# Performance work log

Measured on AMD Instinct MI355X. Metric: run time of the kernel, lower is better.

Reference implementation:

```python
import jax, jax.numpy as jnp
import numpy as np

VOCAB = 10000
EMBED = 100
SEQ = 80
BATCH = 256
UNITS = 2048


def setup_inputs() -> dict:
    key = jax.random.key(0)
    ks = jax.random.split(key, 10)
    s = lambda fan_in: 1.0 / np.sqrt(fan_in)
    inputs = jax.random.randint(ks[0], (BATCH, SEQ), 0, VOCAB, dtype=jnp.int32)
    emb = jax.random.normal(ks[1], (VOCAB, EMBED), dtype=jnp.float32) * 0.05
    W0 = jax.random.normal(ks[2], (EMBED, UNITS), dtype=jnp.float32) * s(EMBED)
    U0 = jax.random.normal(ks[3], (UNITS, UNITS), dtype=jnp.float32) * s(UNITS)
    b0 = jnp.zeros((UNITS,), dtype=jnp.float32)
    W1 = jax.random.normal(ks[4], (UNITS, UNITS), dtype=jnp.float32) * s(UNITS)
    U1 = jax.random.normal(ks[5], (UNITS, UNITS), dtype=jnp.float32) * s(UNITS)
    b1 = jnp.zeros((UNITS,), dtype=jnp.float32)
    Wo = jax.random.normal(ks[6], (UNITS, 1), dtype=jnp.float32) * s(UNITS)
    bo = jnp.zeros((1,), dtype=jnp.float32)
    return {"inputs": inputs, "emb": emb, "W0": W0, "U0": U0, "b0": b0,
            "W1": W1, "U1": U1, "b1": b1, "Wo": Wo, "bo": bo}


def reference(inputs, emb, W0, U0, b0, W1, U1, b1, Wo, bo):
    # Embedding lookup: [B, T, E]
    x = emb[inputs]
    # time-major for scan: [T, B, E]
    xt = jnp.transpose(x, (1, 0, 2))
    B = inputs.shape[0]
    h0_init = jnp.zeros((B, U0.shape[0]), dtype=x.dtype)
    h1_init = jnp.zeros((B, U1.shape[0]), dtype=x.dtype)

    def step(carry, x_t):
        h0, h1 = carry
        # SimpleRNNCell: h' = tanh(x W + h U + b); dropout inactive (training=None)
        h0 = jnp.tanh(x_t @ W0 + h0 @ U0 + b0)
        h1 = jnp.tanh(h0 @ W1 + h1 @ U1 + b1)
        return (h0, h1), None

    (_, h1_final), _ = jax.lax.scan(step, (h0_init, h1_init), xt)
    logits = h1_final @ Wo + bo  # [B, 1]
    return jax.nn.sigmoid(logits)
```

## Files before the change

kernel.cpp:

```cpp
#include <hip/hip_runtime.h>


typedef _Float16 f16;
typedef _Float16 f16x2 __attribute__((ext_vector_type(2)));
typedef _Float16 f16x8 __attribute__((ext_vector_type(8)));
typedef float    f32x4 __attribute__((ext_vector_type(4)));

#define NWG    256
#define SEQ    80
#define EPAD   128
#define NKC0   68
#define NKC1   128

#define FLAGS_OFF   0
#define B0S_OFF     1024
#define B0S_SIZE    (2176 * 2048 * 2)
#define B1S_OFF     (B0S_OFF + B0S_SIZE)
#define B1S_SIZE    (4096 * 2048 * 2)
#define XP_OFF      (B1S_OFF + B1S_SIZE)
#define XP_SIZE     (SEQ * 256 * EPAD * 2)
#define H0_OFF      (XP_OFF + XP_SIZE)
#define HSLOT       (256 * 2048 * 2)
#define HSLOT_H     (256 * 2048)
#define WS_FULL     ((size_t)H0_OFF + (size_t)162 * HSLOT)
#define WS_MIN      ((size_t)H0_OFF + (size_t)6 * HSLOT)

__device__ __forceinline__ float tanh_fast(float x) {
  x = fminf(15.f, fmaxf(-15.f, x));
  float e = __expf(2.f * x);
  return (e - 1.f) * __builtin_amdgcn_rcpf(e + 1.f);
}

__device__ __forceinline__ f16x8 ldg16_coh(const f16* p) {
  f16x8 r;
  asm volatile("global_load_dwordx4 %0, %1, off sc0 sc1" : "=v"(r) : "v"(p));
  return r;
}
__device__ __forceinline__ f16x8 ldg16(const f16* p) {
  f16x8 r;
  asm volatile("global_load_dwordx4 %0, %1, off" : "=v"(r) : "v"(p));
  return r;
}
__device__ __forceinline__ void stg16_coh(f16* p, f16x8 v) {
  asm volatile("global_store_dwordx4 %0, %1, off sc0 sc1" :: "v"(p), "v"(v) : "memory");
}
#define VWAIT(name, n)                                                        \
__device__ __forceinline__ void name(f16x8 (&a)[4], f16x8 (&b)[4]) {          \
  asm volatile("s_waitcnt vmcnt(" #n ")"                                      \
    : "+v"(a[0]), "+v"(a[1]), "+v"(a[2]), "+v"(a[3]),                         \
      "+v"(b[0]), "+v"(b[1]), "+v"(b[2]), "+v"(b[3]) :: "memory");            \
}
VWAIT(vwait16, 16)
VWAIT(vwait8, 8)
VWAIT(vwait0, 0)

__device__ __forceinline__ void gbar(int* flags, int target) {
  asm volatile("s_waitcnt vmcnt(0)" ::: "memory");
  __syncthreads();
  if (threadIdx.x == 0)
    __hip_atomic_store(&flags[blockIdx.x], target, __ATOMIC_RELAXED,
                       __HIP_MEMORY_SCOPE_AGENT);
  if (threadIdx.x < NWG) {
    while (__hip_atomic_load(&flags[threadIdx.x], __ATOMIC_RELAXED,
                             __HIP_MEMORY_SCOPE_AGENT) < target)
      __builtin_amdgcn_s_sleep(2);
  }
  __syncthreads();
}

__global__ __launch_bounds__(256) void fmt_weights(
    const float* __restrict__ W0, const float* __restrict__ U0,
    const float* __restrict__ W1, const float* __restrict__ U1,
    char* __restrict__ ws)
{
  int frag = blockIdx.x * 4 + (threadIdx.x >> 6);
  int lane = threadIdx.x & 63, lr = lane & 15, lk = (lane >> 4) * 8;
  f16x8 h;
  f16* dst;
  if (frag < 32 * NKC0 * 4) {
    int slice = frag / (NKC0 * 4), rem = frag % (NKC0 * 4);
    int kcg = rem >> 2, n16 = rem & 3;
    int col = slice * 64 + n16 * 16 + lr;
#pragma unroll
    for (int j = 0; j < 8; ++j) {
      int k = kcg * 32 + lk + j;
      float v;
      if (k < 2048) v = U0[(size_t)k * 2048 + col];
      else { int e = k - 2048; v = (e < 100) ? W0[(size_t)e * 2048 + col] : 0.f; }
      h[j] = (f16)v;
    }
    dst = (f16*)(ws + B0S_OFF) + (size_t)frag * 512;
  } else {
    int fr = frag - 32 * NKC0 * 4;
    int slice = fr / (NKC1 * 4), rem = fr % (NKC1 * 4);
    int kcg = rem >> 2, n16 = rem & 3;
    int col = slice * 64 + n16 * 16 + lr;
#pragma unroll
    for (int j = 0; j < 8; ++j) {
      int k = kcg * 32 + lk + j;
      float v = (k < 2048) ? W1[(size_t)k * 2048 + col]
                           : U1[(size_t)(k - 2048) * 2048 + col];
      h[j] = (f16)v;
    }
    dst = (f16*)(ws + B1S_OFF) + (size_t)fr * 512;
  }
  *(f16x8*)(dst + lane * 8) = h;
}

__global__ __launch_bounds__(256) void embed_k(
    const int* __restrict__ inputs, const float* __restrict__ emb,
    char* __restrict__ ws)
{
  int r = blockIdx.x * 4 + (threadIdx.x >> 6);
  int lane = threadIdx.x & 63;
  int t = r >> 8, b = r & 255;
  int idx = inputs[b * SEQ + t];
  int e = lane * 2;
  f16x2 h;
  if (e < 100) {
    const float* src = emb + (size_t)idx * 100 + e;
    h[0] = (f16)src[0]; h[1] = (f16)src[1];
  } else { h[0] = (f16)0.f; h[1] = (f16)0.f; }
  *(f16x2*)(ws + XP_OFF + ((size_t)r * EPAD + e) * 2) = h;
}

template <int NKC, bool L0T, bool COH>
__device__ __forceinline__ void ktile(
    const f16* __restrict__ Ab, const f16* __restrict__ Xp,
    const f16* __restrict__ bp, const size_t* aoff, const size_t* xoff,
    int kb, f32x4 (&acc)[4][4])
{
  f16x8 A[3][4], B[3][4];
  auto LD = [&](int kc, f16x8 (&a)[4], f16x8 (&b)[4]) {
#pragma unroll
    for (int cf = 0; cf < 4; ++cf)
      b[cf] = ldg16(bp + (size_t)kc * 2048 + cf * 512);
    int kk = kb + kc * 32;
    if (L0T && kk >= 2048) {
#pragma unroll
      for (int rf = 0; rf < 4; ++rf)
        a[rf] = ldg16(Xp + xoff[rf] + (kk - 2048));
    } else {
#pragma unroll
      for (int rf = 0; rf < 4; ++rf) {
        const f16* p = Ab + aoff[rf] + kk;
        if (COH) a[rf] = ldg16_coh(p); else a[rf] = ldg16(p);
      }
    }
  };
  auto ST = [&](f16x8 (&a)[4], f16x8 (&b)[4]) {
#pragma unroll
    for (int cf = 0; cf < 4; ++cf)
#pragma unroll
      for (int rf = 0; rf < 4; ++rf)
        acc[rf][cf] = __builtin_amdgcn_mfma_f32_16x16x32_f16(
            a[rf], b[cf], acc[rf][cf], 0, 0, 0);
  };

  LD(0, A[0], B[0]);
  if (NKC > 1) LD(1, A[1], B[1]);
#pragma unroll
  for (int kc = 0; kc < NKC; ++kc) {
    f16x8 (&a)[4] = A[kc % 3];
    f16x8 (&b)[4] = B[kc % 3];
    if (kc + 2 < NKC) { LD(kc + 2, A[(kc + 2) % 3], B[(kc + 2) % 3]); vwait16(a, b); }
    else if (kc + 1 < NKC) vwait8(a, b);
    else vwait0(a, b);
    ST(a, b);
  }
}

template <int NBUF, bool COH>
__global__ __launch_bounds__(512, 2) void rnn_persist(
    const float* __restrict__ b0v, const float* __restrict__ b1v,
    char* __restrict__ ws)
{
  __shared__ f32x4 red[8][8][64];
  __shared__ f16 T[64 * 64];

  const int bid = blockIdx.x;
  const int tid = threadIdx.x;
  const int wv = tid >> 6, lane = tid & 63;
  const int lr = lane & 15, lk = (lane >> 4) * 8;

  int* flags = (int*)(ws + FLAGS_OFF);
  f16* H0b = (f16*)(ws + H0_OFF);
  f16* H1b = H0b + (size_t)NBUF * HSLOT_H;
  const f16* Xp = (const f16*)(ws + XP_OFF);

  const bool isL0 = bid < 128;
  const int u = isL0 ? bid : bid - 128;
  const int cslice = (u & 7) * 4 + ((u >> 3) & 3);
  const int m0 = (u >> 5) * 64;
  const int n0 = cslice * 64;
  const f16* Bst = (const f16*)(ws + (isL0 ? B0S_OFF : B1S_OFF));
  const int kcgb = isL0 ? wv * 9 : wv * 16;
  const float* bias = isL0 ? b0v : b1v;

  const f16* bp = Bst + ((size_t)cslice * (isL0 ? NKC0 : NKC1) + kcgb) * 2048 + lane * 8;

  size_t aoff[4], xoff[4];
#pragma unroll
  for (int rf = 0; rf < 4; ++rf)
    aoff[rf] = (size_t)(m0 + rf * 16 + lr) * 2048 + lk;

  for (int p = 0; p <= 80; ++p) {
    const f16* Hr0 = H0b + (size_t)(p % NBUF) * HSLOT_H;
    const f16* Hr1 = H1b + (size_t)((p >= 1 ? (p - 1) % NBUF : 0)) * HSLOT_H;
    f16* Hw = isL0 ? H0b + (size_t)((p + 1) % NBUF) * HSLOT_H
                   : H1b + (size_t)(p % NBUF) * HSLOT_H;
    const bool active = isL0 ? (p < 80) : true;
    const bool fzero  = (!isL0) && (p == 0);

    f32x4 acc[4][4];
#pragma unroll
    for (int a = 0; a < 4; ++a)
#pragma unroll
      for (int b = 0; b < 4; ++b) acc[a][b] = {0.f, 0.f, 0.f, 0.f};

    if (active && !fzero) {
      if (isL0) {
#pragma unroll
        for (int rf = 0; rf < 4; ++rf)
          xoff[rf] = ((size_t)p * 256 + m0 + rf * 16 + lr) * EPAD + lk;
        if (wv < 7) ktile<9, true, COH>(Hr0, Xp, bp, aoff, xoff, wv * 288, acc);
        else        ktile<5, true, COH>(Hr0, Xp, bp, aoff, xoff, wv * 288, acc);
      } else {
        const f16* Ab = (wv < 4) ? Hr0 : Hr1;
        ktile<16, false, COH>(Ab, Xp, bp, aoff, xoff, (wv & 3) * 512, acc);
      }
    }

    if (active) {
#pragma unroll
      for (int t = 0; t < 2; ++t) {
        if (t) __syncthreads();
#pragma unroll
        for (int rr = 0; rr < 2; ++rr)
#pragma unroll
          for (int cf = 0; cf < 4; ++cf)
            red[wv][rr * 4 + cf][lane] = acc[2 * t + rr][cf];
        __syncthreads();
        {
          const int rf = 2 * t + (wv >> 2), cf = wv & 3;
          f32x4 s = red[0][wv][lane];
#pragma unroll
          for (int ow = 1; ow < 8; ++ow) s += red[ow][wv][lane];
          const int tcol = cf * 16 + lr;
          const float bv = bias[n0 + tcol];
          const int trow = rf * 16 + (lane >> 4) * 4;
#pragma unroll
          for (int r = 0; r < 4; ++r) {
            const float v = fzero ? 0.f : tanh_fast(s[r] + bv);
            T[(trow + r) * 64 + (tcol ^ (((trow + r) & 3) << 4))] = (f16)v;
          }
        }
      }
      __syncthreads();
      {
        const int row = tid >> 3, c8 = (tid & 7) * 8;
        f16x8 val = *(const f16x8*)(T + row * 64 + (c8 ^ ((row & 3) << 4)));
        stg16_coh(Hw + (size_t)(m0 + row) * 2048 + n0 + c8, val);
      }
    }
    if (p < 80) gbar(flags, p + 1);
  }
}

__global__ __launch_bounds__(256) void logits_k(
    const f16* __restrict__ h1, const float* __restrict__ Wo,
    const float* __restrict__ bo, float* __restrict__ out)
{
  int row = blockIdx.x * 4 + (threadIdx.x >> 6);
  int lane = threadIdx.x & 63;
  const f16* hr = h1 + (size_t)row * 2048;
  float s = 0.f;
#pragma unroll
  for (int it = 0; it < 4; ++it) {
    int k = it * 512 + lane * 8;
    f16x8 hv = *(const f16x8*)(hr + k);
    const float4* wp = (const float4*)(Wo + k);
    float4 w0 = wp[0], w1 = wp[1];
    s += (float)hv[0] * w0.x + (float)hv[1] * w0.y + (float)hv[2] * w0.z + (float)hv[3] * w0.w;
    s += (float)hv[4] * w1.x + (float)hv[5] * w1.y + (float)hv[6] * w1.z + (float)hv[7] * w1.w;
  }
#pragma unroll
  for (int off = 32; off > 0; off >>= 1) s += __shfl_down(s, off);
  if (lane == 0) out[row] = 1.f / (1.f + __expf(-(s + bo[0])));
}

extern "C" void kernel_launch(void* const* d_in, const int* in_sizes, int n_in,
                              void* d_out, int out_size, void* d_ws, size_t ws_size,
                              hipStream_t stream)
{
  (void)in_sizes; (void)n_in; (void)out_size;
  const int*   inputs = (const int*)d_in[0];
  const float* emb    = (const float*)d_in[1];
  const float* W0     = (const float*)d_in[2];
  const float* U0     = (const float*)d_in[3];
  const float* b0     = (const float*)d_in[4];
  const float* W1     = (const float*)d_in[5];
  const float* U1     = (const float*)d_in[6];
  const float* b1     = (const float*)d_in[7];
  const float* Wo     = (const float*)d_in[8];
  const float* bo     = (const float*)d_in[9];
  char* ws = (char*)d_ws;
  if (ws_size < WS_MIN) return;

  const bool full = (ws_size >= WS_FULL);
  const int  nbuf = full ? 81 : 3;

  hipMemsetAsync(ws + FLAGS_OFF, 0, 1024, stream);
  hipMemsetAsync(ws + H0_OFF, 0, HSLOT, stream);
  hipMemsetAsync(ws + H0_OFF + (size_t)nbuf * HSLOT, 0, HSLOT, stream);

  fmt_weights<<<6272, 256, 0, stream>>>(W0, U0, W1, U1, ws);
  embed_k<<<5120, 256, 0, stream>>>(inputs, emb, ws);
  if (full) rnn_persist<81, false><<<NWG, 512, 0, stream>>>(b0, b1, ws);
  else      rnn_persist<3,  true ><<<NWG, 512, 0, stream>>>(b0, b1, ws);

  const f16* h1f = (const f16*)(ws + H0_OFF + (size_t)nbuf * HSLOT
                                + (size_t)(80 % nbuf) * HSLOT);
  logits_k<<<64, 256, 0, stream>>>(h1f, Wo, bo, (float*)d_out);
}
```

Measured before the change: 2.875 ms.

## Keep per-workgroup weight slices resident in LDS and drop cross-wave reduction

Each workgroup now owns a 16-column output slice over the full K range and preloads its whole weight slice into 128 KB of shared memory once, instead of streaming weights from global memory every timestep. Each wave computes 32 batch rows over the full K, which removes the LDS cross-wave reduction and its extra barriers. The cost is that every workgroup reads the entire hidden state each step, so L2 traffic for activations rises. Outputs are written as scattered 2-byte coherent stores, and occupancy drops to one block per CU.

```diff
diff --git a/kernel.cpp b/kernel.cpp
--- a/kernel.cpp
+++ b/kernel.cpp
@@ -14,9 +14,9 @@
 
 #define FLAGS_OFF   0
 #define B0S_OFF     1024
-#define B0S_SIZE    (2176 * 2048 * 2)
+#define B0S_SIZE    (8704 * 1024)
 #define B1S_OFF     (B0S_OFF + B0S_SIZE)
-#define B1S_SIZE    (4096 * 2048 * 2)
+#define B1S_SIZE    (16384 * 1024)
 #define XP_OFF      (B1S_OFF + B1S_SIZE)
 #define XP_SIZE     (SEQ * 256 * EPAD * 2)
 #define H0_OFF      (XP_OFF + XP_SIZE)
@@ -44,14 +44,18 @@
 __device__ __forceinline__ void stg16_coh(f16* p, f16x8 v) {
   asm volatile("global_store_dwordx4 %0, %1, off sc0 sc1" :: "v"(p), "v"(v) : "memory");
 }
+__device__ __forceinline__ void stg2_coh(f16* p, f16 v) {
+  unsigned int w = (unsigned int)__builtin_bit_cast(unsigned short, v);
+  asm volatile("global_store_short %0, %1, off sc0 sc1" :: "v"(p), "v"(w) : "memory");
+}
 #define VWAIT(name, n)                                                        \
-__device__ __forceinline__ void name(f16x8 (&a)[4], f16x8 (&b)[4]) {          \
+__device__ __forceinline__ void name(f16x8 (&a)[2]) {                         \
   asm volatile("s_waitcnt vmcnt(" #n ")"                                      \
-    : "+v"(a[0]), "+v"(a[1]), "+v"(a[2]), "+v"(a[3]),                         \
-      "+v"(b[0]), "+v"(b[1]), "+v"(b[2]), "+v"(b[3]) :: "memory");            \
-}
-VWAIT(vwait16, 16)
-VWAIT(vwait8, 8)
+    : "+v"(a[0]), "+v"(a[1]) :: "memory");                                    \
+}
+VWAIT(vwait6, 6)
+VWAIT(vwait4, 4)
+VWAIT(vwait2, 2)
 VWAIT(vwait0, 0)
 
 __device__ __forceinline__ void gbar(int* flags, int target) {
@@ -77,13 +81,12 @@
   int lane = threadIdx.x & 63, lr = lane & 15, lk = (lane >> 4) * 8;
   f16x8 h;
   f16* dst;
-  if (frag < 32 * NKC0 * 4) {
-    int slice = frag / (NKC0 * 4), rem = frag % (NKC0 * 4);
-    int kcg = rem >> 2, n16 = rem & 3;
-    int col = slice * 64 + n16 * 16 + lr;
+  if (frag < 128 * NKC0) {
+    int slice = frag / NKC0, kc = frag % NKC0;
+    int col = slice * 16 + lr;
 #pragma unroll
     for (int j = 0; j < 8; ++j) {
-      int k = kcg * 32 + lk + j;
+      int k = kc * 32 + lk + j;
       float v;
       if (k < 2048) v = U0[(size_t)k * 2048 + col];
       else { int e = k - 2048; v = (e < 100) ? W0[(size_t)e * 2048 + col] : 0.f; }
@@ -91,18 +94,17 @@
     }
     dst = (f16*)(ws + B0S_OFF) + (size_t)frag * 512;
   } else {
-    int fr = frag - 32 * NKC0 * 4;
-    int slice = fr / (NKC1 * 4), rem = fr % (NKC1 * 4);
-    int kcg = rem >> 2, n16 = rem & 3;
-    int col = slice * 64 + n16 * 16 + lr;
+    int g2 = frag - 128 * NKC0;
+    int kc = g2 & 127;
+    int col = (g2 >> 7) * 16 + lr;
 #pragma unroll
     for (int j = 0; j < 8; ++j) {
-      int k = kcg * 32 + lk + j;
+      int k = kc * 32 + lk + j;
       float v = (k < 2048) ? W1[(size_t)k * 2048 + col]
                            : U1[(size_t)(k - 2048) * 2048 + col];
       h[j] = (f16)v;
     }
-    dst = (f16*)(ws + B1S_OFF) + (size_t)fr * 512;
+    dst = (f16*)(ws + B1S_OFF) + (size_t)g2 * 512;
   }
   *(f16x8*)(dst + lane * 8) = h;
 }
@@ -124,59 +126,43 @@
   *(f16x2*)(ws + XP_OFF + ((size_t)r * EPAD + e) * 2) = h;
 }
 
-template <int NKC, bool L0T, bool COH>
-__device__ __forceinline__ void ktile(
-    const f16* __restrict__ Ab, const f16* __restrict__ Xp,
-    const f16* __restrict__ bp, const size_t* aoff, const size_t* xoff,
-    int kb, f32x4 (&acc)[4][4])
-{
-  f16x8 A[3][4], B[3][4];
-  auto LD = [&](int kc, f16x8 (&a)[4], f16x8 (&b)[4]) {
-#pragma unroll
-    for (int cf = 0; cf < 4; ++cf)
-      b[cf] = ldg16(bp + (size_t)kc * 2048 + cf * 512);
-    int kk = kb + kc * 32;
-    if (L0T && kk >= 2048) {
-#pragma unroll
-      for (int rf = 0; rf < 4; ++rf)
-        a[rf] = ldg16(Xp + xoff[rf] + (kk - 2048));
-    } else {
-#pragma unroll
-      for (int rf = 0; rf < 4; ++rf) {
-        const f16* p = Ab + aoff[rf] + kk;
-        if (COH) a[rf] = ldg16_coh(p); else a[rf] = ldg16(p);
-      }
-    }
-  };
-  auto ST = [&](f16x8 (&a)[4], f16x8 (&b)[4]) {
-#pragma unroll
-    for (int cf = 0; cf < 4; ++cf)
-#pragma unroll
-      for (int rf = 0; rf < 4; ++rf)
-        acc[rf][cf] = __builtin_amdgcn_mfma_f32_16x16x32_f16(
-            a[rf], b[cf], acc[rf][cf], 0, 0, 0);
-  };
-
-  LD(0, A[0], B[0]);
-  if (NKC > 1) LD(1, A[1], B[1]);
-#pragma unroll
-  for (int kc = 0; kc < NKC; ++kc) {
-    f16x8 (&a)[4] = A[kc % 3];
-    f16x8 (&b)[4] = B[kc % 3];
-    if (kc + 2 < NKC) { LD(kc + 2, A[(kc + 2) % 3], B[(kc + 2) % 3]); vwait16(a, b); }
-    else if (kc + 1 < NKC) vwait8(a, b);
-    else vwait0(a, b);
-    ST(a, b);
-  }
-}
+#define KLOOP(NKC, A1, A2, O1, O2)                                            \
+  do {                                                                        \
+    f16x8 A_[4][2];                                                           \
+    auto LD = [&](int kc, f16x8 (&a)[2]) {                                    \
+      _Pragma("unroll")                                                       \
+      for (int mf = 0; mf < 2; ++mf) {                                        \
+        const f16* p = (kc < 64) ? (A1) + (O1)[mf] + (size_t)kc * 32          \
+                                 : (A2) + (O2)[mf] + (size_t)(kc - 64) * 32;  \
+        if (COH) a[mf] = ldg16_coh(p); else a[mf] = ldg16(p);                 \
+      }                                                                       \
+    };                                                                        \
+    auto STEP = [&](int kc, f16x8 (&a)[2]) {                                  \
+      f16x8 b = Bsh[kc * 64 + lane];                                          \
+      acc[0] = __builtin_amdgcn_mfma_f32_16x16x32_f16(a[0], b, acc[0], 0, 0, 0); \
+      acc[1] = __builtin_amdgcn_mfma_f32_16x16x32_f16(a[1], b, acc[1], 0, 0, 0); \
+    };                                                                        \
+    LD(0, A_[0]); LD(1, A_[1]); LD(2, A_[2]);                                 \
+    for (int kq = 0; kq < (NKC) / 4 - 1; ++kq) {                              \
+      const int k0 = kq * 4;                                                  \
+      LD(k0 + 3, A_[3]); vwait6(A_[0]); STEP(k0 + 0, A_[0]);                  \
+      LD(k0 + 4, A_[0]); vwait6(A_[1]); STEP(k0 + 1, A_[1]);                  \
+      LD(k0 + 5, A_[1]); vwait6(A_[2]); STEP(k0 + 2, A_[2]);                  \
+      LD(k0 + 6, A_[2]); vwait6(A_[3]); STEP(k0 + 3, A_[3]);                  \
+    }                                                                         \
+    LD((NKC) - 1, A_[3]);                                                     \
+    vwait6(A_[0]); STEP((NKC) - 4, A_[0]);                                    \
+    vwait4(A_[1]); STEP((NKC) - 3, A_[1]);                                    \
+    vwait2(A_[2]); STEP((NKC) - 2, A_[2]);                                    \
+    vwait0(A_[3]); STEP((NKC) - 1, A_[3]);                                    \
+  } while (0)
 
 template <int NBUF, bool COH>
-__global__ __launch_bounds__(512, 2) void rnn_persist(
+__global__ __launch_bounds__(512, 1) void rnn_persist(
     const float* __restrict__ b0v, const float* __restrict__ b1v,
     char* __restrict__ ws)
 {
-  __shared__ f32x4 red[8][8][64];
-  __shared__ f16 T[64 * 64];
+  __shared__ f16x8 Bsh[8192];
 
   const int bid = blockIdx.x;
   const int tid = threadIdx.x;
@@ -189,20 +175,23 @@
   const f16* Xp = (const f16*)(ws + XP_OFF);
 
   const bool isL0 = bid < 128;
-  const int u = isL0 ? bid : bid - 128;
-  const int cslice = (u & 7) * 4 + ((u >> 3) & 3);
-  const int m0 = (u >> 5) * 64;
-  const int n0 = cslice * 64;
-  const f16* Bst = (const f16*)(ws + (isL0 ? B0S_OFF : B1S_OFF));
-  const int kcgb = isL0 ? wv * 9 : wv * 16;
+  const int n0 = (isL0 ? bid : bid - 128) * 16;
   const float* bias = isL0 ? b0v : b1v;
 
-  const f16* bp = Bst + ((size_t)cslice * (isL0 ? NKC0 : NKC1) + kcgb) * 2048 + lane * 8;
-
-  size_t aoff[4], xoff[4];
-#pragma unroll
-  for (int rf = 0; rf < 4; ++rf)
-    aoff[rf] = (size_t)(m0 + rf * 16 + lr) * 2048 + lk;
+  {
+    const f16x8* src = (const f16x8*)(isL0
+        ? ws + B0S_OFF + (size_t)bid * (NKC0 * 1024)
+        : ws + B1S_OFF + (size_t)(bid - 128) * (NKC1 * 1024));
+    const int nfr = (isL0 ? NKC0 : NKC1) * 64;
+    for (int i = tid; i < nfr; i += 512) Bsh[i] = src[i];
+    asm volatile("s_waitcnt vmcnt(0)" ::: "memory");
+    __syncthreads();
+  }
+
+  size_t o1[2], xoff[2];
+#pragma unroll
+  for (int mf = 0; mf < 2; ++mf)
+    o1[mf] = (size_t)(wv * 32 + mf * 16 + lr) * 2048 + lk;
 
   for (int p = 0; p <= 80; ++p) {
     const f16* Hr0 = H0b + (size_t)(p % NBUF) * HSLOT_H;
@@ -212,55 +201,31 @@
     const bool active = isL0 ? (p < 80) : true;
     const bool fzero  = (!isL0) && (p == 0);
 
-    f32x4 acc[4][4];
-#pragma unroll
-    for (int a = 0; a < 4; ++a)
-#pragma unroll
-      for (int b = 0; b < 4; ++b) acc[a][b] = {0.f, 0.f, 0.f, 0.f};
-
-    if (active && !fzero) {
-      if (isL0) {
-#pragma unroll
-        for (int rf = 0; rf < 4; ++rf)
-          xoff[rf] = ((size_t)p * 256 + m0 + rf * 16 + lr) * EPAD + lk;
-        if (wv < 7) ktile<9, true, COH>(Hr0, Xp, bp, aoff, xoff, wv * 288, acc);
-        else        ktile<5, true, COH>(Hr0, Xp, bp, aoff, xoff, wv * 288, acc);
-      } else {
-        const f16* Ab = (wv < 4) ? Hr0 : Hr1;
-        ktile<16, false, COH>(Ab, Xp, bp, aoff, xoff, (wv & 3) * 512, acc);
-      }
-    }
-
     if (active) {
-#pragma unroll
-      for (int t = 0; t < 2; ++t) {
-        if (t) __syncthreads();
-#pragma unroll
-        for (int rr = 0; rr < 2; ++rr)
-#pragma unroll
-          for (int cf = 0; cf < 4; ++cf)
-            red[wv][rr * 4 + cf][lane] = acc[2 * t + rr][cf];
-        __syncthreads();
-        {
-          const int rf = 2 * t + (wv >> 2), cf = wv & 3;
-          f32x4 s = red[0][wv][lane];
-#pragma unroll
-          for (int ow = 1; ow < 8; ++ow) s += red[ow][wv][lane];
-          const int tcol = cf * 16 + lr;
-          const float bv = bias[n0 + tcol];
-          const int trow = rf * 16 + (lane >> 4) * 4;
-#pragma unroll
-          for (int r = 0; r < 4; ++r) {
-            const float v = fzero ? 0.f : tanh_fast(s[r] + bv);
-            T[(trow + r) * 64 + (tcol ^ (((trow + r) & 3) << 4))] = (f16)v;
-          }
+      f32x4 acc[2];
+      acc[0] = {0.f, 0.f, 0.f, 0.f};
+      acc[1] = {0.f, 0.f, 0.f, 0.f};
+
+      if (!fzero) {
+        if (isL0) {
+#pragma unroll
+          for (int mf = 0; mf < 2; ++mf)
+            xoff[mf] = ((size_t)p * 256 + wv * 32 + mf * 16 + lr) * EPAD + lk;
+          KLOOP(NKC0, Hr0, Xp, o1, xoff);
+        } else {
+          KLOOP(NKC1, Hr0, Hr1, o1, o1);
         }
       }
-      __syncthreads();
-      {
-        const int row = tid >> 3, c8 = (tid & 7) * 8;
-        f16x8 val = *(const f16x8*)(T + row * 64 + (c8 ^ ((row & 3) << 4)));
-        stg16_coh(Hw + (size_t)(m0 + row) * 2048 + n0 + c8, val);
+
+      const float bv = bias[n0 + lr];
+#pragma unroll
+      for (int mf = 0; mf < 2; ++mf) {
+        const int rb = wv * 32 + mf * 16 + (lane >> 4) * 4;
+#pragma unroll
+        for (int r = 0; r < 4; ++r) {
+          f16 hv = fzero ? (f16)0.f : (f16)tanh_fast(acc[mf][r] + bv);
+          stg2_coh(Hw + (size_t)(rb + r) * 2048 + n0 + lr, hv);
+        }
       }
     }
     if (p < 80) gbar(flags, p + 1);
@@ -319,7 +284,7 @@
   if (full) rnn_persist<81, false><<<NWG, 512, 0, stream>>>(b0, b1, ws);
   else      rnn_persist<3,  true ><<<NWG, 512, 0, stream>>>(b0, b1, ws);
 
-  const f16* h1f = (const f16*)(ws + H0_OFF + (size_t)nbuf * HSLOT
-                                + (size_t)(80 % nbuf) * HSLOT);
+  const f16* h1f = (const f16*)(ws + H0_OFF) + (size_t)nbuf * HSLOT_H
+                   + (size_t)(80 % nbuf) * HSLOT_H;
   logits_k<<<64, 256, 0, stream>>>(h1f, Wo, bo, (float*)d_out);
 }
```

Measured after the change: 5.349 ms. 86.0% more time.
